# Kernel tuning notes

Measured on AMD Instinct MI355X. Metric: run time of the kernel, lower is better.

## Reference

```python
import jax, jax.numpy as jnp
import numpy as np

N = 50000
E = 1600000
D_IN = 768
NHID = 256
NCLASS = 2


def _spmm(rows, cols, vals, dense):
    # out[i] = sum_{e: rows[e]==i} vals[e] * dense[cols[e]]
    return jax.ops.segment_sum(vals[:, None] * dense[cols], rows, num_segments=N)


def _att_fusion(x1, x2, x3, w):
    # a: [N,3] -> abs -> softmax over the 3 branches
    a = jnp.abs(jnp.concatenate([x1, x2, x3], axis=-1) @ w)
    a = jax.nn.softmax(a, axis=-1)  # [N,3]
    x = jnp.stack([x1, x2, x3], axis=-1)  # [N,H,3]
    return jnp.sum(x * a[:, None, :], axis=-1)  # [N,H]


def setup_inputs() -> dict:
    key = jax.random.key(0)
    ks = jax.random.split(key, 24)

    def u(k, shape, fan):
        s = 1.0 / np.sqrt(fan)
        return jax.random.uniform(k, shape, jnp.float32, -s, s)

    inp = {
        "x": jax.random.normal(ks[0], (N, D_IN), jnp.float32),
        "adj_rows": jax.random.randint(ks[1], (E,), 0, N, jnp.int32),
        "adj_cols": jax.random.randint(ks[2], (E,), 0, N, jnp.int32),
        "adj_vals": jax.random.uniform(ks[3], (E,), jnp.float32),
        "s_rows": jax.random.randint(ks[4], (E,), 0, N, jnp.int32),
        "s_cols": jax.random.randint(ks[5], (E,), 0, N, jnp.int32),
        "s_vals": jax.random.uniform(ks[6], (E,), jnp.float32),
        "W1r1": u(ks[7], (D_IN, NHID), NHID),
        "b1r1": u(ks[8], (NHID,), NHID),
        "W1r2": u(ks[9], (D_IN, NHID), NHID),
        "b1r2": u(ks[10], (NHID,), NHID),
        "mlp1_W": u(ks[11], (D_IN, NHID), D_IN),
        "mlp1_b": u(ks[12], (NHID,), D_IN),
        "af1_w": u(ks[13], (3 * NHID, 3), 3 * NHID),
        "W2r1": u(ks[14], (NHID, NCLASS), NCLASS),
        "b2r1": u(ks[15], (NCLASS,), NCLASS),
        "W2r2": u(ks[16], (NHID, NCLASS), NCLASS),
        "b2r2": u(ks[17], (NCLASS,), NCLASS),
        "mlp2_W": u(ks[18], (NHID, NCLASS), NHID),
        "mlp2_b": u(ks[19], (NCLASS,), NHID),
    }
    return inp


def reference(x, adj_rows, adj_cols, adj_vals, s_rows, s_cols, s_vals,
              W1r1, b1r1, W1r2, b1r2, mlp1_W, mlp1_b, af1_w,
              W2r1, b2r1, W2r2, b2r2, mlp2_W, mlp2_b):
    # dropout in eval mode -> identity
    # layer 1: two sparse GCN branches + tanh MLP branch, attention fused
    x_r1 = _spmm(adj_rows, adj_cols, adj_vals, x @ W1r1) + b1r1
    x_r2 = _spmm(s_rows, s_cols, s_vals, x @ W1r2) + b1r2
    x_1 = jnp.tanh(x @ mlp1_W + mlp1_b)
    x1 = _att_fusion(x_r1, x_r2, x_1, af1_w)  # [N, NHID]

    # layer 2: summed branches
    y_r1 = _spmm(adj_rows, adj_cols, adj_vals, x1 @ W2r1) + b2r1
    y_r2 = _spmm(s_rows, s_cols, s_vals, x1 @ W2r2) + b2r2
    y_1 = jnp.tanh(x1 @ mlp2_W + mlp2_b)
    return y_r2 + y_r1 + y_1  # [N, NCLASS]
```

## Files before the change

kernel.cpp:

```cpp
#include <hip/hip_runtime.h>
#include <hip/hip_bf16.h>

#define NN 50000
#define EE 1600000
#define DIN 768
#define NH 256

typedef unsigned short u16;
typedef unsigned int u32;

typedef __attribute__((ext_vector_type(8))) short short8;
typedef __attribute__((ext_vector_type(4))) float f32x4;

__device__ __forceinline__ float bf2f(u16 u) {
  union { u32 i; float f; } x; x.i = ((u32)u) << 16; return x.f;
}
__device__ __forceinline__ u16 f2bf(float f) {
  union { float f; u32 u; } x; x.f = f;
  u32 r = x.u + 0x7fff + ((x.u >> 16) & 1);
  return (u16)(r >> 16);
}

__global__ __launch_bounds__(256) void prep_kernel(
    const float* __restrict__ X, u16* __restrict__ Xb,
    const int* __restrict__ rA, const int* __restrict__ rB,
    int* __restrict__ cntA, int* __restrict__ cntB,
    const float* __restrict__ Wa, const float* __restrict__ Wb,
    const float* __restrict__ Wc, u16* __restrict__ Wt) {
  int b = blockIdx.x;
  if (b < 37500) {
    size_t idx = (size_t)b * 256 + threadIdx.x;
    float4 v = reinterpret_cast<const float4*>(X)[idx];
    ushort4 o;
    o.x = f2bf(v.x); o.y = f2bf(v.y); o.z = f2bf(v.z); o.w = f2bf(v.w);
    reinterpret_cast<ushort4*>(Xb)[idx] = o;
  } else if (b < 50000) {
    int e = (b - 37500) * 256 + threadIdx.x;
    if (e < EE) atomicAdd(&cntA[rA[e]], 1);
    else        atomicAdd(&cntB[rB[e - EE]], 1);
  } else {
    int idx = (b - 50000) * 256 + threadIdx.x;
    int n = idx / DIN, k = idx - n * DIN;
    const float* W = (n < 256) ? Wa : (n < 512) ? Wb : Wc;
    Wt[idx] = f2bf(W[(size_t)k * NH + (n & 255)]);
  }
}

__global__ __launch_bounds__(256) void scan1(int* __restrict__ cntA, int* __restrict__ rsA,
                                             int* __restrict__ cntB, int* __restrict__ rsB,
                                             int* __restrict__ bsum) {
  int* cnt = (blockIdx.y == 0) ? cntA : cntB;
  int* rs  = (blockIdx.y == 0) ? rsA  : rsB;
  int* bs  = bsum + blockIdx.y * 98;
  __shared__ int wsum[4];
  int t = threadIdx.x, lane = t & 63, wid = t >> 6;
  int i0 = blockIdx.x * 512 + 2 * t;
  int v0 = (i0 < NN) ? cnt[i0] : 0;
  int v1 = (i0 + 1 < NN) ? cnt[i0 + 1] : 0;
  int s = v0 + v1;
  int sc = s;
#pragma unroll
  for (int off = 1; off < 64; off <<= 1) {
    int tv = __shfl_up(sc, off, 64);
    if (lane >= off) sc += tv;
  }
  if (lane == 63) wsum[wid] = sc;
  __syncthreads();
  int woff = 0;
  for (int w = 0; w < wid; ++w) woff += wsum[w];
  int excl = woff + sc - s;
  if (i0 < NN)     { cnt[i0] = excl;          rs[i0 + 1] = excl + v0; }
  if (i0 + 1 < NN) { cnt[i0 + 1] = excl + v0; rs[i0 + 2] = excl + v0 + v1; }
  if (t == 255) bs[blockIdx.x] = woff + sc;
  if (blockIdx.x == 0 && t == 0) rs[0] = 0;
}

__global__ __launch_bounds__(128) void scan2(int* __restrict__ bsum) {
  int* bs = bsum + blockIdx.y * 98;
  __shared__ int tmp[128];
  int t = threadIdx.x;
  int orig = (t < 98) ? bs[t] : 0;
  tmp[t] = orig;
  __syncthreads();
  for (int off = 1; off < 128; off <<= 1) {
    int v = (t >= off) ? tmp[t - off] : 0;
    __syncthreads();
    tmp[t] += v;
    __syncthreads();
  }
  if (t < 98) bs[t] = tmp[t] - orig;
}

__global__ __launch_bounds__(512) void scan3(int* __restrict__ cntA, int* __restrict__ rsA,
                                             int* __restrict__ cntB, int* __restrict__ rsB,
                                             const int* __restrict__ bsum) {
  int* cnt = (blockIdx.y == 0) ? cntA : cntB;
  int* rs  = (blockIdx.y == 0) ? rsA  : rsB;
  int off = bsum[blockIdx.y * 98 + blockIdx.x];
  int i = blockIdx.x * 512 + threadIdx.x;
  if (i < NN) { cnt[i] += off; rs[i + 1] += off; }
}

#define TM 128
#define TN 128
#define TK 32
#define GEMM_BLKS 2346
#define TOT_BLKS (GEMM_BLKS + 12500)

__device__ __forceinline__ void gload16(const u16* g, u16* lds) {
  __builtin_amdgcn_global_load_lds((const __attribute__((address_space(1))) unsigned int*)g,
                                   (__attribute__((address_space(3))) unsigned int*)lds, 16, 0, 0);
}

__global__ __launch_bounds__(256) void gemm_scatter(
    const u16* __restrict__ Xb, const u16* __restrict__ Wt, const float* __restrict__ mlp1_b,
    u16* __restrict__ H1, u16* __restrict__ H2, u16* __restrict__ T,
    const int* __restrict__ rA, const int* __restrict__ cA, const float* __restrict__ vA,
    const int* __restrict__ rB, const int* __restrict__ cB, const float* __restrict__ vB,
    int* __restrict__ curA, int2* __restrict__ edgeA,
    int* __restrict__ curB, int2* __restrict__ edgeB) {
  __shared__ u16 As[TM * TK];
  __shared__ u16 Bs[TN * TK];

  const int b = blockIdx.x;
  const int lo = (b * GEMM_BLKS) / TOT_BLKS;
  const int hi = ((b + 1) * GEMM_BLKS) / TOT_BLKS;

  if (hi > lo) {
    const int gid = lo;
    const int tid = threadIdx.x;
    const int lane = tid & 63;
    const int w = tid >> 6;
    const int n0 = (gid % 6) * TN;
    const int m0 = (gid / 6) * TM;
    const int wm = w >> 1, wn = w & 1;

    f32x4 acc[4][4] = {};

    const int r_l = lane >> 2;
    const int kcp = lane & 3;
    const int r16 = lane & 15;
    const int kcl = lane >> 4;

    for (int k0 = 0; k0 < DIN; k0 += TK) {
#pragma unroll
      for (int q = 0; q < 2; ++q) {
        int row = w * 32 + q * 16 + r_l;
        int kc = kcp ^ ((row >> 1) & 3);
        int gr = m0 + row; if (gr >= NN) gr = NN - 1;
        gload16(Xb + (size_t)gr * DIN + k0 + kc * 8, &As[(w * 32 + q * 16) * TK]);
        gload16(Wt + (size_t)(n0 + row) * DIN + k0 + kc * 8, &Bs[(w * 32 + q * 16) * TK]);
      }
      __syncthreads();

      short8 aF[4], bF[4];
#pragma unroll
      for (int i = 0; i < 4; ++i) {
        int m = wm * 64 + i * 16 + r16;
        aF[i] = *reinterpret_cast<const short8*>(&As[m * TK + (kcl ^ ((m >> 1) & 3)) * 8]);
        int n = wn * 64 + i * 16 + r16;
        bF[i] = *reinterpret_cast<const short8*>(&Bs[n * TK + (kcl ^ ((n >> 1) & 3)) * 8]);
      }
#pragma unroll
      for (int i = 0; i < 4; ++i)
#pragma unroll
        for (int j = 0; j < 4; ++j)
          acc[i][j] = __builtin_amdgcn_mfma_f32_16x16x32_bf16(aF[i], bF[j], acc[i][j], 0, 0, 0);
      __syncthreads();
    }

    const int bsel = n0 >> 8;
    u16* O = (bsel == 0) ? H1 : (bsel == 1) ? H2 : T;
    const int act = (bsel == 2);
    const int cb = n0 & 255;
    const int rq = lane >> 4;
#pragma unroll
    for (int i = 0; i < 4; ++i) {
#pragma unroll
      for (int r = 0; r < 4; ++r) {
        int grow = m0 + wm * 64 + i * 16 + rq * 4 + r;
        if (grow >= NN) continue;
#pragma unroll
        for (int j = 0; j < 4; ++j) {
          int c = cb + wn * 64 + j * 16 + r16;
          float v = acc[i][j][r];
          if (act) v = tanhf(v + mlp1_b[c]);
          O[(size_t)grow * NH + c] = f2bf(v);
        }
      }
    }
  } else {
    const int sid = b - lo;
    int e = sid * 256 + threadIdx.x;
    if (e < EE) {
      int r = rA[e];
      int p = atomicAdd(&curA[r], 1);
      int2 o; o.x = cA[e]; o.y = __float_as_int(vA[e]);
      edgeA[p] = o;
    } else {
      e -= EE;
      int r = rB[e];
      int p = atomicAdd(&curB[r], 1);
      int2 o; o.x = cB[e]; o.y = __float_as_int(vB[e]);
      edgeB[p] = o;
    }
  }
}

__global__ __launch_bounds__(256) void spmm_h2(
    const int* __restrict__ rsA, const int2* __restrict__ edgeA,
    const u16* __restrict__ HA, const float* __restrict__ biasA, u16* __restrict__ outA,
    const int* __restrict__ rsB, const int2* __restrict__ edgeB,
    const u16* __restrict__ HB, const float* __restrict__ biasB, u16* __restrict__ outB) {
  const int* rs; const int2* edge; const u16* H; const float* bias; u16* out;
  if (blockIdx.y == 0) { rs = rsA; edge = edgeA; H = HA; bias = biasA; out = outA; }
  else                 { rs = rsB; edge = edgeB; H = HB; bias = biasB; out = outB; }

  int tid = threadIdx.x, lane = tid & 63, w = tid >> 6;
  int n = blockIdx.x * 4 + w;
  int h0 = (lane & 31) * 8;
  int eg = lane >> 5;
  int s = rs[n], e = rs[n + 1];
  float acc[8] = {};
  int i = s + eg;
  for (; i + 2 < e; i += 4) {
    int2 e0 = edge[i], e1 = edge[i + 2];
    float v0 = __int_as_float(e0.y), v1 = __int_as_float(e1.y);
    short8 hv0 = *reinterpret_cast<const short8*>(H + (size_t)e0.x * NH + h0);
    short8 hv1 = *reinterpret_cast<const short8*>(H + (size_t)e1.x * NH + h0);
#pragma unroll
    for (int j = 0; j < 8; ++j) acc[j] += v0 * bf2f((u16)hv0[j]);
#pragma unroll
    for (int j = 0; j < 8; ++j) acc[j] += v1 * bf2f((u16)hv1[j]);
  }
  if (i < e) {
    int2 e0 = edge[i];
    float v0 = __int_as_float(e0.y);
    short8 hv0 = *reinterpret_cast<const short8*>(H + (size_t)e0.x * NH + h0);
#pragma unroll
    for (int j = 0; j < 8; ++j) acc[j] += v0 * bf2f((u16)hv0[j]);
  }
#pragma unroll
  for (int j = 0; j < 8; ++j) acc[j] += __shfl_xor(acc[j], 32, 64);
  if (eg == 0) {
    float4 b0 = *reinterpret_cast<const float4*>(bias + h0);
    float4 b1 = *reinterpret_cast<const float4*>(bias + h0 + 4);
    float bb[8] = {b0.x, b0.y, b0.z, b0.w, b1.x, b1.y, b1.z, b1.w};
    short8 o;
#pragma unroll
    for (int j = 0; j < 8; ++j) o[j] = (short)f2bf(acc[j] + bb[j]);
    *reinterpret_cast<short8*>(out + (size_t)n * NH + h0) = o;
  }
}

__global__ __launch_bounds__(256) void fuse_l2(
    const u16* __restrict__ R1, const u16* __restrict__ R2, const u16* __restrict__ T,
    const float* __restrict__ afw,
    const float* __restrict__ W2r1, const float* __restrict__ W2r2,
    const float* __restrict__ mlpW, const float* __restrict__ mlpb,
    float* __restrict__ Z1, float* __restrict__ Z2, float* __restrict__ Y1) {
  __shared__ float w[DIN * 3];
  __shared__ float w1[NH * 2], w2[NH * 2], wm[NH * 2];
  int tid = threadIdx.x;
  for (int i = tid; i < DIN * 3; i += 256) w[i] = afw[i];
  for (int i = tid; i < NH * 2; i += 256) { w1[i] = W2r1[i]; w2[i] = W2r2[i]; wm[i] = mlpW[i]; }
  __syncthreads();
  int lane = tid & 63, wave = tid >> 6;
  int n = blockIdx.x * 4 + wave;
  int h0 = lane * 4;
  ushort4 r1v = *reinterpret_cast<const ushort4*>(R1 + (size_t)n * NH + h0);
  ushort4 r2v = *reinterpret_cast<const ushort4*>(R2 + (size_t)n * NH + h0);
  ushort4 tv  = *reinterpret_cast<const ushort4*>(T  + (size_t)n * NH + h0);
  float r1[4] = {bf2f(r1v.x), bf2f(r1v.y), bf2f(r1v.z), bf2f(r1v.w)};
  float r2[4] = {bf2f(r2v.x), bf2f(r2v.y), bf2f(r2v.z), bf2f(r2v.w)};
  float t[4]  = {bf2f(tv.x),  bf2f(tv.y),  bf2f(tv.z),  bf2f(tv.w)};
  float l0 = 0.f, l1 = 0.f, l2 = 0.f;
#pragma unroll
  for (int i = 0; i < 4; ++i) {
    int h = h0 + i;
    l0 += r1[i] * w[h * 3 + 0] + r2[i] * w[(NH + h) * 3 + 0] + t[i] * w[(2 * NH + h) * 3 + 0];
    l1 += r1[i] * w[h * 3 + 1] + r2[i] * w[(NH + h) * 3 + 1] + t[i] * w[(2 * NH + h) * 3 + 1];
    l2 += r1[i] * w[h * 3 + 2] + r2[i] * w[(NH + h) * 3 + 2] + t[i] * w[(2 * NH + h) * 3 + 2];
  }
#pragma unroll
  for (int off = 32; off > 0; off >>= 1) {
    l0 += __shfl_xor(l0, off, 64);
    l1 += __shfl_xor(l1, off, 64);
    l2 += __shfl_xor(l2, off, 64);
  }
  l0 = fabsf(l0); l1 = fabsf(l1); l2 = fabsf(l2);
  float m = fmaxf(l0, fmaxf(l1, l2));
  float e0 = expf(l0 - m), e1 = expf(l1 - m), e2 = expf(l2 - m);
  float inv = 1.f / (e0 + e1 + e2);
  float a0 = e0 * inv, a1 = e1 * inv, a2 = e2 * inv;

  float p10 = 0.f, p11 = 0.f, p20 = 0.f, p21 = 0.f, p30 = 0.f, p31 = 0.f;
#pragma unroll
  for (int i = 0; i < 4; ++i) {
    int h = h0 + i;
    float xv = a0 * r1[i] + a1 * r2[i] + a2 * t[i];
    p10 += xv * w1[h * 2 + 0]; p11 += xv * w1[h * 2 + 1];
    p20 += xv * w2[h * 2 + 0]; p21 += xv * w2[h * 2 + 1];
    p30 += xv * wm[h * 2 + 0]; p31 += xv * wm[h * 2 + 1];
  }
#pragma unroll
  for (int off = 32; off > 0; off >>= 1) {
    p10 += __shfl_down(p10, off, 64); p11 += __shfl_down(p11, off, 64);
    p20 += __shfl_down(p20, off, 64); p21 += __shfl_down(p21, off, 64);
    p30 += __shfl_down(p30, off, 64); p31 += __shfl_down(p31, off, 64);
  }
  if (lane == 0) {
    Z1[n * 2 + 0] = p10; Z1[n * 2 + 1] = p11;
    Z2[n * 2 + 0] = p20; Z2[n * 2 + 1] = p21;
    Y1[n * 2 + 0] = tanhf(p30 + mlpb[0]);
    Y1[n * 2 + 1] = tanhf(p31 + mlpb[1]);
  }
}

__global__ __launch_bounds__(256) void spmm2_final(
    const int* __restrict__ rsA, const int2* __restrict__ edgeA,
    const int* __restrict__ rsB, const int2* __restrict__ edgeB,
    const float* __restrict__ Z1, const float* __restrict__ Z2, const float* __restrict__ Y1,
    const float* __restrict__ b2r1, const float* __restrict__ b2r2,
    float* __restrict__ out) {
  int tid = threadIdx.x;
  int lane = tid & 63, wave = tid >> 6;
  int n = blockIdx.x * 4 + wave;
  float a0 = 0.f, a1 = 0.f;
  {
    int s = rsA[n], e = rsA[n + 1];
    for (int i = s + lane; i < e; i += 64) {
      int2 ed = edgeA[i];
      float v = __int_as_float(ed.y);
      float2 z = *reinterpret_cast<const float2*>(Z1 + ed.x * 2);
      a0 += v * z.x; a1 += v * z.y;
    }
  }
  float c0 = 0.f, c1 = 0.f;
  {
    int s = rsB[n], e = rsB[n + 1];
    for (int i = s + lane; i < e; i += 64) {
      int2 ed = edgeB[i];
      float v = __int_as_float(ed.y);
      float2 z = *reinterpret_cast<const float2*>(Z2 + ed.x * 2);
      c0 += v * z.x; c1 += v * z.y;
    }
  }
#pragma unroll
  for (int off = 32; off > 0; off >>= 1) {
    a0 += __shfl_down(a0, off, 64); a1 += __shfl_down(a1, off, 64);
    c0 += __shfl_down(c0, off, 64); c1 += __shfl_down(c1, off, 64);
  }
  if (lane == 0) {
    out[n * 2 + 0] = (a0 + b2r1[0]) + (c0 + b2r2[0]) + Y1[n * 2 + 0];
    out[n * 2 + 1] = (a1 + b2r1[1]) + (c1 + b2r2[1]) + Y1[n * 2 + 1];
  }
}

extern "C" void kernel_launch(void* const* d_in, const int* in_sizes, int n_in,
                              void* d_out, int out_size, void* d_ws, size_t ws_size,
                              hipStream_t stream) {
  const float* x        = (const float*)d_in[0];
  const int*   adj_rows = (const int*)d_in[1];
  const int*   adj_cols = (const int*)d_in[2];
  const float* adj_vals = (const float*)d_in[3];
  const int*   s_rows   = (const int*)d_in[4];
  const int*   s_cols   = (const int*)d_in[5];
  const float* s_vals   = (const float*)d_in[6];
  const float* W1r1     = (const float*)d_in[7];
  const float* b1r1     = (const float*)d_in[8];
  const float* W1r2     = (const float*)d_in[9];
  const float* b1r2     = (const float*)d_in[10];
  const float* mlp1_W   = (const float*)d_in[11];
  const float* mlp1_b   = (const float*)d_in[12];
  const float* af1_w    = (const float*)d_in[13];
  const float* W2r1     = (const float*)d_in[14];
  const float* b2r1     = (const float*)d_in[15];
  const float* W2r2     = (const float*)d_in[16];
  const float* b2r2     = (const float*)d_in[17];
  const float* mlp2_W   = (const float*)d_in[18];
  const float* mlp2_b   = (const float*)d_in[19];
  float* out = (float*)d_out;

  char* p = (char*)d_ws;
  auto alloc = [&](size_t b) { char* r = p; p += (b + 255) & ~(size_t)255; return r; };

  char* xb_region = alloc((size_t)NN * DIN * 2);
  u16* Xb = (u16*)xb_region;
  u16* R1 = (u16*)xb_region;
  u16* R2 = (u16*)(xb_region + (size_t)NN * NH * 2);
  char* zreg = xb_region + (size_t)2 * NN * NH * 2;
  float* Z1 = (float*)zreg;
  float* Z2 = (float*)(zreg + (size_t)NN * 2 * 4);
  float* Y1 = (float*)(zreg + (size_t)NN * 4 * 4);

  u16* H1 = (u16*)alloc((size_t)NN * NH * 2);
  u16* H2 = (u16*)alloc((size_t)NN * NH * 2);
  u16* T  = (u16*)alloc((size_t)NN * NH * 2);
  u16* Wt = (u16*)alloc((size_t)DIN * DIN * 2);
  int*  rsA   = (int*)alloc((size_t)(NN + 1) * 4);
  int*  curA  = (int*)alloc((size_t)NN * 4);
  int2* edgeA = (int2*)alloc((size_t)EE * 8);
  int*  rsB   = (int*)alloc((size_t)(NN + 1) * 4);
  int*  curB  = (int*)alloc((size_t)NN * 4);
  int2* edgeB = (int2*)alloc((size_t)EE * 8);
  int*  bsum  = (int*)alloc(2 * 98 * 4);

  hipMemsetAsync(curA, 0, (size_t)NN * 4, stream);
  hipMemsetAsync(curB, 0, (size_t)NN * 4, stream);
  prep_kernel<<<52304, 256, 0, stream>>>(x, Xb, adj_rows, s_rows, curA, curB,
                                         W1r1, W1r2, mlp1_W, Wt);

  dim3 gsc(98, 2);
  scan1<<<gsc, 256, 0, stream>>>(curA, rsA, curB, rsB, bsum);
  scan2<<<dim3(1, 2), 128, 0, stream>>>(bsum);
  scan3<<<gsc, 512, 0, stream>>>(curA, rsA, curB, rsB, bsum);

  gemm_scatter<<<TOT_BLKS, 256, 0, stream>>>(Xb, Wt, mlp1_b, H1, H2, T,
                                             adj_rows, adj_cols, adj_vals,
                                             s_rows, s_cols, s_vals,
                                             curA, edgeA, curB, edgeB);

  dim3 gs(12500, 2);
  spmm_h2<<<gs, 256, 0, stream>>>(rsA, edgeA, H1, b1r1, R1,
                                  rsB, edgeB, H2, b1r2, R2);

  fuse_l2<<<NN / 4, 256, 0, stream>>>(R1, R2, T, af1_w, W2r1, W2r2, mlp2_W, mlp2_b,
                                      Z1, Z2, Y1);

  spmm2_final<<<NN / 4, 256, 0, stream>>>(rsA, edgeA, rsB, edgeB,
                                          Z1, Z2, Y1, b2r1, b2r2, out);
}
```

Before: 943.1 us.

## Fuse layer-1 SpMM with attention fusion and partition CSR scatter by row slice

```diff
diff --git a/kernel.cpp b/kernel.cpp
--- a/kernel.cpp
+++ b/kernel.cpp
@@ -105,7 +105,9 @@
 #define TN 128
 #define TK 32
 #define GEMM_BLKS 2346
-#define TOT_BLKS (GEMM_BLKS + 12500)
+#define NUNITS 1563
+#define CHUNK 2048
+#define TOT_BLKS (NUNITS * 16)
 
 __device__ __forceinline__ void gload16(const u16* g, u16* lds) {
   __builtin_amdgcn_global_load_lds((const __attribute__((address_space(1))) unsigned int*)g,
@@ -123,11 +125,12 @@
   __shared__ u16 Bs[TN * TK];
 
   const int b = blockIdx.x;
-  const int lo = (b * GEMM_BLKS) / TOT_BLKS;
-  const int hi = ((b + 1) * GEMM_BLKS) / TOT_BLKS;
-
-  if (hi > lo) {
-    const int gid = lo;
+  const int u = b >> 4;
+  const int r = b & 15;
+
+  if (r >= 8) {
+    const int gid = u * 8 + (r - 8);
+    if (gid >= GEMM_BLKS) return;
     const int tid = threadIdx.x;
     const int lane = tid & 63;
     const int w = tid >> 6;
@@ -177,137 +180,170 @@
 #pragma unroll
     for (int i = 0; i < 4; ++i) {
 #pragma unroll
-      for (int r = 0; r < 4; ++r) {
-        int grow = m0 + wm * 64 + i * 16 + rq * 4 + r;
+      for (int rr = 0; rr < 4; ++rr) {
+        int grow = m0 + wm * 64 + i * 16 + rq * 4 + rr;
         if (grow >= NN) continue;
 #pragma unroll
         for (int j = 0; j < 4; ++j) {
           int c = cb + wn * 64 + j * 16 + r16;
-          float v = acc[i][j][r];
+          float v = acc[i][j][rr];
           if (act) v = tanhf(v + mlp1_b[c]);
           O[(size_t)grow * NH + c] = f2bf(v);
         }
       }
     }
   } else {
-    const int sid = b - lo;
-    int e = sid * 256 + threadIdx.x;
-    if (e < EE) {
-      int r = rA[e];
-      int p = atomicAdd(&curA[r], 1);
-      int2 o; o.x = cA[e]; o.y = __float_as_int(vA[e]);
-      edgeA[p] = o;
-    } else {
-      e -= EE;
-      int r = rB[e];
-      int p = atomicAdd(&curB[r], 1);
-      int2 o; o.x = cB[e]; o.y = __float_as_int(vB[e]);
-      edgeB[p] = o;
-    }
-  }
-}
-
-__global__ __launch_bounds__(256) void spmm_h2(
+    const int slice = r;
+    const int base = u * CHUNK;
+    for (int t = threadIdx.x; t < CHUNK; t += 256) {
+      int e = base + t;
+      if (e < EE) {
+        int rw = rA[e];
+        if ((rw & 7) == slice) {
+          int p = atomicAdd(&curA[rw], 1);
+          int2 o; o.x = cA[e]; o.y = __float_as_int(vA[e]);
+          edgeA[p] = o;
+        }
+      } else if (e < 2 * EE) {
+        int e2 = e - EE;
+        int rw = rB[e2];
+        if ((rw & 7) == slice) {
+          int p = atomicAdd(&curB[rw], 1);
+          int2 o; o.x = cB[e2]; o.y = __float_as_int(vB[e2]);
+          edgeB[p] = o;
+        }
+      }
+    }
+  }
+}
+
+__global__ __launch_bounds__(256) void spmm_fuse(
     const int* __restrict__ rsA, const int2* __restrict__ edgeA,
-    const u16* __restrict__ HA, const float* __restrict__ biasA, u16* __restrict__ outA,
+    const u16* __restrict__ H1, const float* __restrict__ b1,
     const int* __restrict__ rsB, const int2* __restrict__ edgeB,
-    const u16* __restrict__ HB, const float* __restrict__ biasB, u16* __restrict__ outB) {
-  const int* rs; const int2* edge; const u16* H; const float* bias; u16* out;
-  if (blockIdx.y == 0) { rs = rsA; edge = edgeA; H = HA; bias = biasA; out = outA; }
-  else                 { rs = rsB; edge = edgeB; H = HB; bias = biasB; out = outB; }
-
-  int tid = threadIdx.x, lane = tid & 63, w = tid >> 6;
-  int n = blockIdx.x * 4 + w;
-  int h0 = (lane & 31) * 8;
-  int eg = lane >> 5;
-  int s = rs[n], e = rs[n + 1];
-  float acc[8] = {};
-  int i = s + eg;
-  for (; i + 2 < e; i += 4) {
-    int2 e0 = edge[i], e1 = edge[i + 2];
-    float v0 = __int_as_float(e0.y), v1 = __int_as_float(e1.y);
-    short8 hv0 = *reinterpret_cast<const short8*>(H + (size_t)e0.x * NH + h0);
-    short8 hv1 = *reinterpret_cast<const short8*>(H + (size_t)e1.x * NH + h0);
-#pragma unroll
-    for (int j = 0; j < 8; ++j) acc[j] += v0 * bf2f((u16)hv0[j]);
-#pragma unroll
-    for (int j = 0; j < 8; ++j) acc[j] += v1 * bf2f((u16)hv1[j]);
-  }
-  if (i < e) {
-    int2 e0 = edge[i];
-    float v0 = __int_as_float(e0.y);
-    short8 hv0 = *reinterpret_cast<const short8*>(H + (size_t)e0.x * NH + h0);
-#pragma unroll
-    for (int j = 0; j < 8; ++j) acc[j] += v0 * bf2f((u16)hv0[j]);
-  }
-#pragma unroll
-  for (int j = 0; j < 8; ++j) acc[j] += __shfl_xor(acc[j], 32, 64);
-  if (eg == 0) {
-    float4 b0 = *reinterpret_cast<const float4*>(bias + h0);
-    float4 b1 = *reinterpret_cast<const float4*>(bias + h0 + 4);
-    float bb[8] = {b0.x, b0.y, b0.z, b0.w, b1.x, b1.y, b1.z, b1.w};
-    short8 o;
-#pragma unroll
-    for (int j = 0; j < 8; ++j) o[j] = (short)f2bf(acc[j] + bb[j]);
-    *reinterpret_cast<short8*>(out + (size_t)n * NH + h0) = o;
-  }
-}
-
-__global__ __launch_bounds__(256) void fuse_l2(
-    const u16* __restrict__ R1, const u16* __restrict__ R2, const u16* __restrict__ T,
-    const float* __restrict__ afw,
+    const u16* __restrict__ H2, const float* __restrict__ b2,
+    const u16* __restrict__ T, const float* __restrict__ afw,
     const float* __restrict__ W2r1, const float* __restrict__ W2r2,
     const float* __restrict__ mlpW, const float* __restrict__ mlpb,
     float* __restrict__ Z1, float* __restrict__ Z2, float* __restrict__ Y1) {
   __shared__ float w[DIN * 3];
-  __shared__ float w1[NH * 2], w2[NH * 2], wm[NH * 2];
+  __shared__ float w1[NH * 2], w2[NH * 2], wmm[NH * 2];
   int tid = threadIdx.x;
   for (int i = tid; i < DIN * 3; i += 256) w[i] = afw[i];
-  for (int i = tid; i < NH * 2; i += 256) { w1[i] = W2r1[i]; w2[i] = W2r2[i]; wm[i] = mlpW[i]; }
+  for (int i = tid; i < NH * 2; i += 256) { w1[i] = W2r1[i]; w2[i] = W2r2[i]; wmm[i] = mlpW[i]; }
   __syncthreads();
-  int lane = tid & 63, wave = tid >> 6;
-  int n = blockIdx.x * 4 + wave;
-  int h0 = lane * 4;
-  ushort4 r1v = *reinterpret_cast<const ushort4*>(R1 + (size_t)n * NH + h0);
-  ushort4 r2v = *reinterpret_cast<const ushort4*>(R2 + (size_t)n * NH + h0);
-  ushort4 tv  = *reinterpret_cast<const ushort4*>(T  + (size_t)n * NH + h0);
-  float r1[4] = {bf2f(r1v.x), bf2f(r1v.y), bf2f(r1v.z), bf2f(r1v.w)};
-  float r2[4] = {bf2f(r2v.x), bf2f(r2v.y), bf2f(r2v.z), bf2f(r2v.w)};
-  float t[4]  = {bf2f(tv.x),  bf2f(tv.y),  bf2f(tv.z),  bf2f(tv.w)};
+
+  int lane = tid & 63, wv = tid >> 6;
+  int n = blockIdx.x * 4 + wv;
+  int h0 = (lane & 31) * 8;
+  int eg = lane >> 5;
+
+  float ac1[8] = {}, ac2[8] = {};
+  {
+    int s = rsA[n], e = rsA[n + 1];
+    int i = s + eg;
+    for (; i + 6 < e; i += 8) {
+      int2 e0 = edgeA[i], e1 = edgeA[i + 2], e2 = edgeA[i + 4], e3 = edgeA[i + 6];
+      short8 v0 = *reinterpret_cast<const short8*>(H1 + (size_t)e0.x * NH + h0);
+      short8 v1 = *reinterpret_cast<const short8*>(H1 + (size_t)e1.x * NH + h0);
+      short8 v2 = *reinterpret_cast<const short8*>(H1 + (size_t)e2.x * NH + h0);
+      short8 v3 = *reinterpret_cast<const short8*>(H1 + (size_t)e3.x * NH + h0);
+      float f0 = __int_as_float(e0.y), f1 = __int_as_float(e1.y);
+      float f2 = __int_as_float(e2.y), f3 = __int_as_float(e3.y);
+#pragma unroll
+      for (int j = 0; j < 8; ++j)
+        ac1[j] += f0 * bf2f((u16)v0[j]) + f1 * bf2f((u16)v1[j])
+                + f2 * bf2f((u16)v2[j]) + f3 * bf2f((u16)v3[j]);
+    }
+    for (; i < e; i += 2) {
+      int2 e0 = edgeA[i];
+      short8 v0 = *reinterpret_cast<const short8*>(H1 + (size_t)e0.x * NH + h0);
+      float f0 = __int_as_float(e0.y);
+#pragma unroll
+      for (int j = 0; j < 8; ++j) ac1[j] += f0 * bf2f((u16)v0[j]);
+    }
+  }
+  {
+    int s = rsB[n], e = rsB[n + 1];
+    int i = s + eg;
+    for (; i + 6 < e; i += 8) {
+      int2 e0 = edgeB[i], e1 = edgeB[i + 2], e2 = edgeB[i + 4], e3 = edgeB[i + 6];
+      short8 v0 = *reinterpret_cast<const short8*>(H2 + (size_t)e0.x * NH + h0);
+      short8 v1 = *reinterpret_cast<const short8*>(H2 + (size_t)e1.x * NH + h0);
+      short8 v2 = *reinterpret_cast<const short8*>(H2 + (size_t)e2.x * NH + h0);
+      short8 v3 = *reinterpret_cast<const short8*>(H2 + (size_t)e3.x * NH + h0);
+      float f0 = __int_as_float(e0.y), f1 = __int_as_float(e1.y);
+      float f2 = __int_as_float(e2.y), f3 = __int_as_float(e3.y);
+#pragma unroll
+      for (int j = 0; j < 8; ++j)
+        ac2[j] += f0 * bf2f((u16)v0[j]) + f1 * bf2f((u16)v1[j])
+                + f2 * bf2f((u16)v2[j]) + f3 * bf2f((u16)v3[j]);
+    }
+    for (; i < e; i += 2) {
+      int2 e0 = edgeB[i];
+      short8 v0 = *reinterpret_cast<const short8*>(H2 + (size_t)e0.x * NH + h0);
+      float f0 = __int_as_float(e0.y);
+#pragma unroll
+      for (int j = 0; j < 8; ++j) ac2[j] += f0 * bf2f((u16)v0[j]);
+    }
+  }
+#pragma unroll
+  for (int j = 0; j < 8; ++j) {
+    ac1[j] += __shfl_xor(ac1[j], 32, 64);
+    ac2[j] += __shfl_xor(ac2[j], 32, 64);
+  }
+
+  float r1[8], r2[8], t8[8];
+  {
+    float4 bA0 = *reinterpret_cast<const float4*>(b1 + h0);
+    float4 bA1 = *reinterpret_cast<const float4*>(b1 + h0 + 4);
+    float4 bB0 = *reinterpret_cast<const float4*>(b2 + h0);
+    float4 bB1 = *reinterpret_cast<const float4*>(b2 + h0 + 4);
+    float bbA[8] = {bA0.x, bA0.y, bA0.z, bA0.w, bA1.x, bA1.y, bA1.z, bA1.w};
+    float bbB[8] = {bB0.x, bB0.y, bB0.z, bB0.w, bB1.x, bB1.y, bB1.z, bB1.w};
+    short8 tv = *reinterpret_cast<const short8*>(T + (size_t)n * NH + h0);
+#pragma unroll
+    for (int j = 0; j < 8; ++j) {
+      r1[j] = ac1[j] + bbA[j];
+      r2[j] = ac2[j] + bbB[j];
+      t8[j] = bf2f((u16)tv[j]);
+    }
+  }
+
   float l0 = 0.f, l1 = 0.f, l2 = 0.f;
 #pragma unroll
-  for (int i = 0; i < 4; ++i) {
-    int h = h0 + i;
-    l0 += r1[i] * w[h * 3 + 0] + r2[i] * w[(NH + h) * 3 + 0] + t[i] * w[(2 * NH + h) * 3 + 0];
-    l1 += r1[i] * w[h * 3 + 1] + r2[i] * w[(NH + h) * 3 + 1] + t[i] * w[(2 * NH + h) * 3 + 1];
-    l2 += r1[i] * w[h * 3 + 2] + r2[i] * w[(NH + h) * 3 + 2] + t[i] * w[(2 * NH + h) * 3 + 2];
-  }
-#pragma unroll
-  for (int off = 32; off > 0; off >>= 1) {
+  for (int k = 0; k < 8; ++k) {
+    int h = h0 + k;
+    l0 += r1[k] * w[h * 3 + 0] + r2[k] * w[(NH + h) * 3 + 0] + t8[k] * w[(2 * NH + h) * 3 + 0];
+    l1 += r1[k] * w[h * 3 + 1] + r2[k] * w[(NH + h) * 3 + 1] + t8[k] * w[(2 * NH + h) * 3 + 1];
+    l2 += r1[k] * w[h * 3 + 2] + r2[k] * w[(NH + h) * 3 + 2] + t8[k] * w[(2 * NH + h) * 3 + 2];
+  }
+#pragma unroll
+  for (int off = 16; off > 0; off >>= 1) {
     l0 += __shfl_xor(l0, off, 64);
     l1 += __shfl_xor(l1, off, 64);
     l2 += __shfl_xor(l2, off, 64);
   }
   l0 = fabsf(l0); l1 = fabsf(l1); l2 = fabsf(l2);
-  float m = fmaxf(l0, fmaxf(l1, l2));
-  float e0 = expf(l0 - m), e1 = expf(l1 - m), e2 = expf(l2 - m);
+  float mx = fmaxf(l0, fmaxf(l1, l2));
+  float e0 = expf(l0 - mx), e1 = expf(l1 - mx), e2 = expf(l2 - mx);
   float inv = 1.f / (e0 + e1 + e2);
-  float a0 = e0 * inv, a1 = e1 * inv, a2 = e2 * inv;
+  float s0 = e0 * inv, s1 = e1 * inv, s2 = e2 * inv;
 
   float p10 = 0.f, p11 = 0.f, p20 = 0.f, p21 = 0.f, p30 = 0.f, p31 = 0.f;
 #pragma unroll
-  for (int i = 0; i < 4; ++i) {
-    int h = h0 + i;
-    float xv = a0 * r1[i] + a1 * r2[i] + a2 * t[i];
+  for (int k = 0; k < 8; ++k) {
+    int h = h0 + k;
+    float xv = s0 * r1[k] + s1 * r2[k] + s2 * t8[k];
     p10 += xv * w1[h * 2 + 0]; p11 += xv * w1[h * 2 + 1];
     p20 += xv * w2[h * 2 + 0]; p21 += xv * w2[h * 2 + 1];
-    p30 += xv * wm[h * 2 + 0]; p31 += xv * wm[h * 2 + 1];
-  }
-#pragma unroll
-  for (int off = 32; off > 0; off >>= 1) {
-    p10 += __shfl_down(p10, off, 64); p11 += __shfl_down(p11, off, 64);
-    p20 += __shfl_down(p20, off, 64); p21 += __shfl_down(p21, off, 64);
-    p30 += __shfl_down(p30, off, 64); p31 += __shfl_down(p31, off, 64);
+    p30 += xv * wmm[h * 2 + 0]; p31 += xv * wmm[h * 2 + 1];
+  }
+#pragma unroll
+  for (int off = 16; off > 0; off >>= 1) {
+    p10 += __shfl_xor(p10, off, 64); p11 += __shfl_xor(p11, off, 64);
+    p20 += __shfl_xor(p20, off, 64); p21 += __shfl_xor(p21, off, 64);
+    p30 += __shfl_xor(p30, off, 64); p31 += __shfl_xor(p31, off, 64);
   }
   if (lane == 0) {
     Z1[n * 2 + 0] = p10; Z1[n * 2 + 1] = p11;
@@ -387,12 +423,9 @@
 
   char* xb_region = alloc((size_t)NN * DIN * 2);
   u16* Xb = (u16*)xb_region;
-  u16* R1 = (u16*)xb_region;
-  u16* R2 = (u16*)(xb_region + (size_t)NN * NH * 2);
-  char* zreg = xb_region + (size_t)2 * NN * NH * 2;
-  float* Z1 = (float*)zreg;
-  float* Z2 = (float*)(zreg + (size_t)NN * 2 * 4);
-  float* Y1 = (float*)(zreg + (size_t)NN * 4 * 4);
+  float* Z1 = (float*)xb_region;
+  float* Z2 = (float*)(xb_region + (size_t)NN * 2 * 4);
+  float* Y1 = (float*)(xb_region + (size_t)NN * 4 * 4);
 
   u16* H1 = (u16*)alloc((size_t)NN * NH * 2);
   u16* H2 = (u16*)alloc((size_t)NN * NH * 2);
@@ -421,12 +454,10 @@
                                              s_rows, s_cols, s_vals,
                                              curA, edgeA, curB, edgeB);
 
-  dim3 gs(12500, 2);
-  spmm_h2<<<gs, 256, 0, stream>>>(rsA, edgeA, H1, b1r1, R1,
-                                  rsB, edgeB, H2, b1r2, R2);
-
-  fuse_l2<<<NN / 4, 256, 0, stream>>>(R1, R2, T, af1_w, W2r1, W2r2, mlp2_W, mlp2_b,
-                                      Z1, Z2, Y1);
+  spmm_fuse<<<NN / 4, 256, 0, stream>>>(rsA, edgeA, H1, b1r1,
+                                        rsB, edgeB, H2, b1r2,
+                                        T, af1_w, W2r1, W2r2, mlp2_W, mlp2_b,
+                                        Z1, Z2, Y1);
 
   spmm2_final<<<NN / 4, 256, 0, stream>>>(rsA, edgeA, rsB, edgeB,
                                           Z1, Z2, Y1, b2r1, b2r2, out);
```

After: 1.172 ms. 1.24x slower.
